# Optimization experiments

Measured on AMD Instinct MI355X. Metric: run time of the kernel, lower is better.

## Reference

```python
import jax, jax.numpy as jnp
import numpy as np

B, N, T = 32, 256, 1024  # batch, num_dimensions, time_dur


def setup_inputs() -> dict:
    key = jax.random.key(0)
    k1, k2 = jax.random.split(key)
    x = jax.random.normal(k1, (B, N, T), dtype=jnp.float32)
    # DBNN.__init__: tau_rise=50, tau_decay=200, omega=2 (all per-dimension)
    tau_rise = jnp.full((N,), 50.0, dtype=jnp.float32)
    tau_decay = jnp.full((N,), 200.0, dtype=jnp.float32)
    omega = jnp.full((N,), 2.0, dtype=jnp.float32)
    # BilinearModified weight: uniform(-1/sqrt(N), 1/sqrt(N)), shape [out=1, N, N]
    bound = 1.0 / np.sqrt(N)
    W = jax.random.uniform(k2, (1, N, N), minval=-bound, maxval=bound, dtype=jnp.float32)
    return {"x": x, "tau_rise": tau_rise, "tau_decay": tau_decay, "omega": omega, "W": W}


def reference(x, tau_rise, tau_decay, omega, W):
    B_, N_, T_ = x.shape
    BIAS = -70.0  # fixed bias buffer in BilinearModified

    # --- create_kernels: [N, T] exponential rise/decay kernels ---
    t = jnp.arange(T_, dtype=x.dtype)
    kernels = (omega[:, None]
               * (1.0 - jnp.exp(-t / tau_rise[:, None]))
               * jnp.exp(-t / tau_decay[:, None]))  # [N, T]

    # torch flips the kernel then runs cross-correlation (conv1d) => causal convolution
    k_flipped = jnp.flip(kernels, axis=-1)[:, None, :]  # [N, 1, T] (OIW, depthwise)

    y = jax.lax.conv_general_dilated(
        x, k_flipped,
        window_strides=(1,),
        padding=[(T_ - 1, T_ - 1)],
        dimension_numbers=("NCH", "OIH", "NCH"),
        feature_group_count=N_,
    )[:, :, :T_]  # [B, N, T]

    yt = jnp.transpose(y, (0, 2, 1))  # [B, T, N]

    # Bilinear with diagonal of weight zeroed (mask-multiply, equivalent to the
    # in-place diagonal-zeroing loop in the torch module)
    Wm = W * (1.0 - jnp.eye(N_, dtype=W.dtype))  # [1, N, N]
    bilinear = jnp.einsum("btn,onm,btm->bto", yt, Wm, yt)  # [B, T, 1]

    linear = jnp.sum(yt, axis=2, keepdims=True)  # [B, T, 1]
    out = bilinear + BIAS + linear
    return out[..., 0]  # [B, T]
```

## Files before the change

kernel.cpp:

```cpp
#include <hip/hip_runtime.h>

typedef _Float16 f16;
typedef _Float16 f16x4 __attribute__((ext_vector_type(4)));
typedef _Float16 f16x8 __attribute__((ext_vector_type(8)));
typedef float    f32x4 __attribute__((ext_vector_type(4)));

#define NB 32
#define ND 256
#define NT 1024

__global__ __launch_bounds__(256) void iir_wprep_kernel(
    const float* __restrict__ x, const float* __restrict__ tau_rise,
    const float* __restrict__ tau_decay, const float* __restrict__ omega,
    const float* __restrict__ W, f16* __restrict__ y16, f16* __restrict__ wf)
{
    if (blockIdx.x >= 2048) {
        const int gid  = (blockIdx.x - 2048) * 256 + threadIdx.x;
        const int ks8  = gid >> 10;
        const int nt   = (gid >> 6) & 15;
        const int lane = gid & 63;
        const int nrow = nt * 16 + (lane & 15);
        const int k0   = ks8 * 32 + (lane >> 4) * 8;
        f16x8 v;
        #pragma unroll
        for (int j = 0; j < 8; ++j) {
            int k = k0 + j;
            float w = W[nrow * 256 + k];
            v[j] = (f16)((k == nrow) ? 0.0f : w);
        }
        *reinterpret_cast<f16x8*>(wf + (size_t)gid * 8) = v;
        return;
    }

    const int lane = threadIdx.x & 63;
    const int wid  = threadIdx.x >> 6;
    const int row  = blockIdx.x * 4 + wid;
    const int n    = row & (ND - 1);

    const float td = tau_decay[n];
    const float tr = tau_rise[n];
    const float om = omega[n];
    const float ad = expf(-1.0f / td);
    const float am = expf(-(1.0f / tr + 1.0f / td));

    const float* xr = x + (size_t)row * NT + lane * 16;
    float xv[16];
    #pragma unroll
    for (int i = 0; i < 4; ++i) {
        f32x4 v = *reinterpret_cast<const f32x4*>(xr + i * 4);
        xv[i*4+0] = v[0]; xv[i*4+1] = v[1]; xv[i*4+2] = v[2]; xv[i*4+3] = v[3];
    }

    float ld[16], lm[16];
    float sd = 0.f, sm = 0.f;
    #pragma unroll
    for (int i = 0; i < 16; ++i) {
        sd = fmaf(ad, sd, xv[i]); ld[i] = sd;
        sm = fmaf(am, sm, xv[i]); lm[i] = sm;
    }

    float t2;
    t2 = ad * ad; t2 = t2 * t2; t2 = t2 * t2; const float a16d = t2 * t2;
    t2 = am * am; t2 = t2 * t2; t2 = t2 * t2; const float a16m = t2 * t2;

    float Xd = sd, Xm = sm;
    float wdp = a16d, wmp = a16m;
    #pragma unroll
    for (int off = 1; off < 64; off <<= 1) {
        float pd = __shfl_up(Xd, off);
        float pm = __shfl_up(Xm, off);
        if (lane >= off) { Xd = fmaf(wdp, pd, Xd); Xm = fmaf(wmp, pm, Xm); }
        wdp *= wdp; wmp *= wmp;
    }
    float cd = __shfl_up(Xd, 1);
    float cm = __shfl_up(Xm, 1);
    if (lane == 0) { cd = 0.f; cm = 0.f; }

    f16x8 o0, o1;
    float pd = ad, pm = am;
    #pragma unroll
    for (int i = 0; i < 16; ++i) {
        float yd = fmaf(pd, cd, ld[i]);
        float ym = fmaf(pm, cm, lm[i]);
        float yv = om * (yd - ym);
        if (i < 8) o0[i] = (f16)yv; else o1[i - 8] = (f16)yv;
        pd *= ad; pm *= am;
    }
    f16* dst = y16 + (size_t)row * NT + lane * 16;
    *reinterpret_cast<f16x8*>(dst)     = o0;
    *reinterpret_cast<f16x8*>(dst + 8) = o1;
}

__global__ __launch_bounds__(512, 4) void bilinear_kernel(
    const f16* __restrict__ y16, const f16* __restrict__ wf,
    float* __restrict__ out)
{
    __shared__ __align__(16) f16 Yl[16384];
    __shared__ float sbuf[8][64];

    const int bi = blockIdx.x;
    const int tt = bi & 15;
    const int b  = bi >> 4;
    const int t0 = tt * 64;
    const int tid = threadIdx.x;

    {
        const int m    = tid & 255;
        const int half = tid >> 8;
        const f16* ysrc = y16 + ((size_t)(b * ND + m)) * NT + t0 + half * 32;
        f16x8 vy[4];
        #pragma unroll
        for (int c = 0; c < 4; ++c)
            vy[c] = *reinterpret_cast<const f16x8*>(ysrc + c * 8);
        #pragma unroll
        for (int c = 0; c < 4; ++c) {
            #pragma unroll
            for (int e = 0; e < 8; ++e) {
                int tl = half * 32 + c * 8 + e;
                Yl[tl * 256 + (m ^ (e << 3))] = vy[c][e];
            }
        }
    }
    __syncthreads();

    const int lane = tid & 63;
    const int w    = tid >> 6;
    const int g    = lane >> 4;

    int tl4[4], sw4[4];
    #pragma unroll
    for (int tf = 0; tf < 4; ++tf) {
        tl4[tf] = tf * 16 + (lane & 15);
        sw4[tf] = (tl4[tf] & 7) << 3;
    }

    f32x4 acc[2][4];
    #pragma unroll
    for (int a = 0; a < 2; ++a)
        #pragma unroll
        for (int tf = 0; tf < 4; ++tf) acc[a][tf] = (f32x4){0.f,0.f,0.f,0.f};

    #pragma unroll
    for (int ks = 0; ks < 8; ++ks) {
        f16x8 afrag[2];
        #pragma unroll
        for (int a = 0; a < 2; ++a)
            afrag[a] = *reinterpret_cast<const f16x8*>(
                &wf[(size_t)(((ks * 16) + (2 * w + a)) * 64 + lane) * 8]);
        f16x8 bfrag[4];
        #pragma unroll
        for (int tf = 0; tf < 4; ++tf) {
            int m0 = ks * 32 + g * 8;
            bfrag[tf] = *reinterpret_cast<const f16x8*>(
                &Yl[tl4[tf] * 256 + (m0 ^ sw4[tf])]);
        }
        #pragma unroll
        for (int a = 0; a < 2; ++a)
            #pragma unroll
            for (int tf = 0; tf < 4; ++tf)
                acc[a][tf] = __builtin_amdgcn_mfma_f32_16x16x32_f16(
                    afrag[a], bfrag[tf], acc[a][tf], 0, 0, 0);
    }

    #pragma unroll
    for (int tf = 0; tf < 4; ++tf) {
        float p = 0.f;
        #pragma unroll
        for (int a = 0; a < 2; ++a) {
            int n0 = w * 32 + a * 16 + g * 4;
            f16x4 yv4 = *reinterpret_cast<const f16x4*>(
                &Yl[tl4[tf] * 256 + (n0 ^ sw4[tf])]);
            #pragma unroll
            for (int r = 0; r < 4; ++r)
                p = fmaf((float)yv4[r], acc[a][tf][r] + 1.0f, p);
        }
        p += __shfl_xor(p, 16);
        p += __shfl_xor(p, 32);
        if (lane < 16) sbuf[w][tf * 16 + lane] = p;
    }
    __syncthreads();
    if (tid < 64) {
        float s = sbuf[0][tid] + sbuf[1][tid] + sbuf[2][tid] + sbuf[3][tid]
                + sbuf[4][tid] + sbuf[5][tid] + sbuf[6][tid] + sbuf[7][tid];
        out[b * NT + t0 + tid] = s - 70.0f;
    }
}

extern "C" void kernel_launch(void* const* d_in, const int* in_sizes, int n_in,
                              void* d_out, int out_size, void* d_ws, size_t ws_size,
                              hipStream_t stream) {
    const float* x         = (const float*)d_in[0];
    const float* tau_rise  = (const float*)d_in[1];
    const float* tau_decay = (const float*)d_in[2];
    const float* omega     = (const float*)d_in[3];
    const float* W         = (const float*)d_in[4];
    float* out = (float*)d_out;

    f16* y16 = (f16*)d_ws;
    f16* wfr = (f16*)((char*)d_ws + (size_t)16 * 1024 * 1024);

    iir_wprep_kernel<<<2048 + 32, 256, 0, stream>>>(
        x, tau_rise, tau_decay, omega, W, y16, wfr);
    bilinear_kernel<<<NB * 16, 512, 0, stream>>>(y16, wfr, out);
}
```

Baseline: 24.08 us.

## Store scan checkpoints and recompute filtered signal inside bilinear kernel

The first kernel now writes only per-32-step IIR carry checkpoints instead of the full fp16 filtered tensor. The bilinear kernel rereads x in fp32, restarts the recurrence from each checkpoint, and writes the fp16 result straight into shared memory. This drops the 16 MB y16 write and its reread, but x (32 MB) is now read twice. It also adds a 32-step serial recurrence per thread inside the bilinear kernel, with scalar, bank-conflicting shared stores.

```diff
diff --git a/kernel.cpp b/kernel.cpp
--- a/kernel.cpp
+++ b/kernel.cpp
@@ -9,10 +9,11 @@
 #define ND 256
 #define NT 1024
 
-__global__ __launch_bounds__(256) void iir_wprep_kernel(
+__global__ __launch_bounds__(256) void scan_chk_wprep_kernel(
     const float* __restrict__ x, const float* __restrict__ tau_rise,
     const float* __restrict__ tau_decay, const float* __restrict__ omega,
-    const float* __restrict__ W, f16* __restrict__ y16, f16* __restrict__ wf)
+    const float* __restrict__ W, float2* __restrict__ chk,
+    f16* __restrict__ wf)
 {
     if (blockIdx.x >= 2048) {
         const int gid  = (blockIdx.x - 2048) * 256 + threadIdx.x;
@@ -37,62 +38,47 @@
     const int row  = blockIdx.x * 4 + wid;
     const int n    = row & (ND - 1);
 
-    const float td = tau_decay[n];
-    const float tr = tau_rise[n];
-    const float om = omega[n];
-    const float ad = expf(-1.0f / td);
-    const float am = expf(-(1.0f / tr + 1.0f / td));
+    const float ad = expf(-1.0f / tau_decay[n]);
+    const float am = expf(-(1.0f / tau_rise[n] + 1.0f / tau_decay[n]));
 
     const float* xr = x + (size_t)row * NT + lane * 16;
-    float xv[16];
-    #pragma unroll
-    for (int i = 0; i < 4; ++i) {
-        f32x4 v = *reinterpret_cast<const f32x4*>(xr + i * 4);
-        xv[i*4+0] = v[0]; xv[i*4+1] = v[1]; xv[i*4+2] = v[2]; xv[i*4+3] = v[3];
-    }
-
-    float ld[16], lm[16];
+    f32x4 v0 = *reinterpret_cast<const f32x4*>(xr);
+    f32x4 v1 = *reinterpret_cast<const f32x4*>(xr + 4);
+    f32x4 v2 = *reinterpret_cast<const f32x4*>(xr + 8);
+    f32x4 v3 = *reinterpret_cast<const f32x4*>(xr + 12);
+
     float sd = 0.f, sm = 0.f;
     #pragma unroll
-    for (int i = 0; i < 16; ++i) {
-        sd = fmaf(ad, sd, xv[i]); ld[i] = sd;
-        sm = fmaf(am, sm, xv[i]); lm[i] = sm;
-    }
+    for (int i = 0; i < 4; ++i) { sd = fmaf(ad, sd, v0[i]); sm = fmaf(am, sm, v0[i]); }
+    #pragma unroll
+    for (int i = 0; i < 4; ++i) { sd = fmaf(ad, sd, v1[i]); sm = fmaf(am, sm, v1[i]); }
+    #pragma unroll
+    for (int i = 0; i < 4; ++i) { sd = fmaf(ad, sd, v2[i]); sm = fmaf(am, sm, v2[i]); }
+    #pragma unroll
+    for (int i = 0; i < 4; ++i) { sd = fmaf(ad, sd, v3[i]); sm = fmaf(am, sm, v3[i]); }
 
     float t2;
-    t2 = ad * ad; t2 = t2 * t2; t2 = t2 * t2; const float a16d = t2 * t2;
-    t2 = am * am; t2 = t2 * t2; t2 = t2 * t2; const float a16m = t2 * t2;
+    t2 = ad * ad; t2 = t2 * t2; t2 = t2 * t2; float wd = t2 * t2;
+    t2 = am * am; t2 = t2 * t2; t2 = t2 * t2; float wm = t2 * t2;
 
     float Xd = sd, Xm = sm;
-    float wdp = a16d, wmp = a16m;
     #pragma unroll
     for (int off = 1; off < 64; off <<= 1) {
         float pd = __shfl_up(Xd, off);
         float pm = __shfl_up(Xm, off);
-        if (lane >= off) { Xd = fmaf(wdp, pd, Xd); Xm = fmaf(wmp, pm, Xm); }
-        wdp *= wdp; wmp *= wmp;
-    }
-    float cd = __shfl_up(Xd, 1);
-    float cm = __shfl_up(Xm, 1);
-    if (lane == 0) { cd = 0.f; cm = 0.f; }
-
-    f16x8 o0, o1;
-    float pd = ad, pm = am;
-    #pragma unroll
-    for (int i = 0; i < 16; ++i) {
-        float yd = fmaf(pd, cd, ld[i]);
-        float ym = fmaf(pm, cm, lm[i]);
-        float yv = om * (yd - ym);
-        if (i < 8) o0[i] = (f16)yv; else o1[i - 8] = (f16)yv;
-        pd *= ad; pm *= am;
-    }
-    f16* dst = y16 + (size_t)row * NT + lane * 16;
-    *reinterpret_cast<f16x8*>(dst)     = o0;
-    *reinterpret_cast<f16x8*>(dst + 8) = o1;
+        if (lane >= off) { Xd = fmaf(wd, pd, Xd); Xm = fmaf(wm, pm, Xm); }
+        wd *= wd; wm *= wm;
+    }
+
+    float2* cr = chk + (size_t)row * 32;
+    if (lane == 0) cr[0] = make_float2(0.f, 0.f);
+    if ((lane & 1) && lane < 63) cr[(lane + 1) >> 1] = make_float2(Xd, Xm);
 }
 
 __global__ __launch_bounds__(512, 4) void bilinear_kernel(
-    const f16* __restrict__ y16, const f16* __restrict__ wf,
+    const float* __restrict__ x, const float* __restrict__ tau_rise,
+    const float* __restrict__ tau_decay, const float* __restrict__ omega,
+    const float2* __restrict__ chk, const f16* __restrict__ wf,
     float* __restrict__ out)
 {
     __shared__ __align__(16) f16 Yl[16384];
@@ -105,27 +91,36 @@
     const int tid = threadIdx.x;
 
     {
-        const int m    = tid & 255;
-        const int half = tid >> 8;
-        const f16* ysrc = y16 + ((size_t)(b * ND + m)) * NT + t0 + half * 32;
-        f16x8 vy[4];
-        #pragma unroll
-        for (int c = 0; c < 4; ++c)
-            vy[c] = *reinterpret_cast<const f16x8*>(ysrc + c * 8);
-        #pragma unroll
-        for (int c = 0; c < 4; ++c) {
-            #pragma unroll
-            for (int e = 0; e < 8; ++e) {
-                int tl = half * 32 + c * 8 + e;
-                Yl[tl * 256 + (m ^ (e << 3))] = vy[c][e];
-            }
+        const int m = tid >> 1;
+        const int h = tid & 1;
+        const int rowg = b * ND + m;
+        const float ad = expf(-1.0f / tau_decay[m]);
+        const float am = expf(-(1.0f / tau_rise[m] + 1.0f / tau_decay[m]));
+        const float om = omega[m];
+
+        const float* xs = x + (size_t)rowg * NT + t0 + h * 32;
+        f32x4 xv[8];
+        #pragma unroll
+        for (int c = 0; c < 8; ++c)
+            xv[c] = *reinterpret_cast<const f32x4*>(xs + c * 4);
+
+        float2 ck = chk[(size_t)rowg * 32 + tt * 2 + h];
+        float Sd = ck.x, Sm = ck.y;
+        #pragma unroll
+        for (int i = 0; i < 32; ++i) {
+            float xi = xv[i >> 2][i & 3];
+            Sd = fmaf(ad, Sd, xi);
+            Sm = fmaf(am, Sm, xi);
+            float yv = om * (Sd - Sm);
+            int tl = h * 32 + i;
+            Yl[tl * 256 + (m ^ ((tl & 7) << 3))] = (f16)yv;
         }
     }
     __syncthreads();
 
     const int lane = tid & 63;
     const int w    = tid >> 6;
-    const int g    = lane >> 4;
+    const int gq   = lane >> 4;
 
     int tl4[4], sw4[4];
     #pragma unroll
@@ -150,7 +145,7 @@
         f16x8 bfrag[4];
         #pragma unroll
         for (int tf = 0; tf < 4; ++tf) {
-            int m0 = ks * 32 + g * 8;
+            int m0 = ks * 32 + gq * 8;
             bfrag[tf] = *reinterpret_cast<const f16x8*>(
                 &Yl[tl4[tf] * 256 + (m0 ^ sw4[tf])]);
         }
@@ -167,7 +162,7 @@
         float p = 0.f;
         #pragma unroll
         for (int a = 0; a < 2; ++a) {
-            int n0 = w * 32 + a * 16 + g * 4;
+            int n0 = w * 32 + a * 16 + gq * 4;
             f16x4 yv4 = *reinterpret_cast<const f16x4*>(
                 &Yl[tl4[tf] * 256 + (n0 ^ sw4[tf])]);
             #pragma unroll
@@ -196,10 +191,11 @@
     const float* W         = (const float*)d_in[4];
     float* out = (float*)d_out;
 
-    f16* y16 = (f16*)d_ws;
-    f16* wfr = (f16*)((char*)d_ws + (size_t)16 * 1024 * 1024);
-
-    iir_wprep_kernel<<<2048 + 32, 256, 0, stream>>>(
-        x, tau_rise, tau_decay, omega, W, y16, wfr);
-    bilinear_kernel<<<NB * 16, 512, 0, stream>>>(y16, wfr, out);
+    float2* chk = (float2*)d_ws;
+    f16*    wfr = (f16*)((char*)d_ws + (size_t)4 * 1024 * 1024);
+
+    scan_chk_wprep_kernel<<<2048 + 32, 256, 0, stream>>>(
+        x, tau_rise, tau_decay, omega, W, chk, wfr);
+    bilinear_kernel<<<NB * 16, 512, 0, stream>>>(
+        x, tau_rise, tau_decay, omega, chk, wfr, out);
 }
```

After: 24.37 us. Within noise of the previous version (+1.2%).

## Halve bilinear block size, widen per-wave tiles, double-buffer W fragments

Applied to the files above, without the earlier changes.

The bilinear kernel now runs 256 threads per block instead of 512. Each wave computes four 16-row W tiles instead of two, so each Y fragment read from LDS is reused across more MFMAs. The W fragment global loads are double-buffered, prefetching the next k-slice while the current one is multiplied. The Y tile is now staged with 4-wide f16x4 LDS stores that gather four rows per thread. The cost is higher register pressure and fewer waves per block, which may reduce latency hiding.

```diff
diff --git a/kernel.cpp b/kernel.cpp
--- a/kernel.cpp
+++ b/kernel.cpp
@@ -91,12 +91,12 @@
     *reinterpret_cast<f16x8*>(dst + 8) = o1;
 }
 
-__global__ __launch_bounds__(512, 4) void bilinear_kernel(
+__global__ __launch_bounds__(256, 2) void bilinear_kernel(
     const f16* __restrict__ y16, const f16* __restrict__ wf,
     float* __restrict__ out)
 {
     __shared__ __align__(16) f16 Yl[16384];
-    __shared__ float sbuf[8][64];
+    __shared__ float sbuf[4][64];
 
     const int bi = blockIdx.x;
     const int tt = bi & 15;
@@ -105,27 +105,32 @@
     const int tid = threadIdx.x;
 
     {
-        const int m    = tid & 255;
-        const int half = tid >> 8;
-        const f16* ysrc = y16 + ((size_t)(b * ND + m)) * NT + t0 + half * 32;
-        f16x8 vy[4];
-        #pragma unroll
-        for (int c = 0; c < 4; ++c)
-            vy[c] = *reinterpret_cast<const f16x8*>(ysrc + c * 8);
-        #pragma unroll
-        for (int c = 0; c < 4; ++c) {
-            #pragma unroll
-            for (int e = 0; e < 8; ++e) {
-                int tl = half * 32 + c * 8 + e;
-                Yl[tl * 256 + (m ^ (e << 3))] = vy[c][e];
-            }
+        const int j2 = tid & 63;
+        const int h  = tid >> 6;
+        const f16* base = y16 + ((size_t)(b * ND + 4 * j2)) * NT + t0 + h * 16;
+        f16x8 vy[4][2];
+        #pragma unroll
+        for (int r = 0; r < 4; ++r) {
+            vy[r][0] = *reinterpret_cast<const f16x8*>(base + (size_t)r * NT);
+            vy[r][1] = *reinterpret_cast<const f16x8*>(base + (size_t)r * NT + 8);
+        }
+        #pragma unroll
+        for (int i = 0; i < 16; ++i) {
+            const int tl = h * 16 + i;
+            f16x4 v4;
+            v4[0] = vy[0][i >> 3][i & 7];
+            v4[1] = vy[1][i >> 3][i & 7];
+            v4[2] = vy[2][i >> 3][i & 7];
+            v4[3] = vy[3][i >> 3][i & 7];
+            *reinterpret_cast<f16x4*>(
+                &Yl[tl * 256 + ((4 * j2) ^ ((tl & 7) << 3))]) = v4;
         }
     }
     __syncthreads();
 
     const int lane = tid & 63;
     const int w    = tid >> 6;
-    const int g    = lane >> 4;
+    const int gq   = lane >> 4;
 
     int tl4[4], sw4[4];
     #pragma unroll
@@ -134,40 +139,70 @@
         sw4[tf] = (tl4[tf] & 7) << 3;
     }
 
-    f32x4 acc[2][4];
-    #pragma unroll
-    for (int a = 0; a < 2; ++a)
+    f32x4 acc[4][4];
+    #pragma unroll
+    for (int a = 0; a < 4; ++a)
         #pragma unroll
         for (int tf = 0; tf < 4; ++tf) acc[a][tf] = (f32x4){0.f,0.f,0.f,0.f};
 
-    #pragma unroll
-    for (int ks = 0; ks < 8; ++ks) {
-        f16x8 afrag[2];
-        #pragma unroll
-        for (int a = 0; a < 2; ++a)
-            afrag[a] = *reinterpret_cast<const f16x8*>(
-                &wf[(size_t)(((ks * 16) + (2 * w + a)) * 64 + lane) * 8]);
-        f16x8 bfrag[4];
-        #pragma unroll
-        for (int tf = 0; tf < 4; ++tf) {
-            int m0 = ks * 32 + g * 8;
-            bfrag[tf] = *reinterpret_cast<const f16x8*>(
-                &Yl[tl4[tf] * 256 + (m0 ^ sw4[tf])]);
-        }
-        #pragma unroll
-        for (int a = 0; a < 2; ++a)
-            #pragma unroll
-            for (int tf = 0; tf < 4; ++tf)
-                acc[a][tf] = __builtin_amdgcn_mfma_f32_16x16x32_f16(
-                    afrag[a], bfrag[tf], acc[a][tf], 0, 0, 0);
+    const f16* wbase = wf + (size_t)(4 * w) * 512 + (size_t)lane * 8;
+
+    f16x8 aA[4], aB[4];
+    #pragma unroll
+    for (int a_ = 0; a_ < 4; ++a_)
+        aA[a_] = *reinterpret_cast<const f16x8*>(wbase + (size_t)a_ * 512);
+
+    #pragma unroll
+    for (int kp = 0; kp < 4; ++kp) {
+        const int ks0 = 2 * kp, ks1 = 2 * kp + 1;
+        #pragma unroll
+        for (int a_ = 0; a_ < 4; ++a_)
+            aB[a_] = *reinterpret_cast<const f16x8*>(
+                wbase + (size_t)(ks1 * 16 + a_) * 512);
+        {
+            f16x8 bfrag[4];
+            #pragma unroll
+            for (int tf = 0; tf < 4; ++tf) {
+                int m0 = ks0 * 32 + gq * 8;
+                bfrag[tf] = *reinterpret_cast<const f16x8*>(
+                    &Yl[tl4[tf] * 256 + (m0 ^ sw4[tf])]);
+            }
+            #pragma unroll
+            for (int a = 0; a < 4; ++a)
+                #pragma unroll
+                for (int tf = 0; tf < 4; ++tf)
+                    acc[a][tf] = __builtin_amdgcn_mfma_f32_16x16x32_f16(
+                        aA[a], bfrag[tf], acc[a][tf], 0, 0, 0);
+        }
+        if (kp < 3) {
+            #pragma unroll
+            for (int a_ = 0; a_ < 4; ++a_)
+                aA[a_] = *reinterpret_cast<const f16x8*>(
+                    wbase + (size_t)((ks1 + 1) * 16 + a_) * 512);
+        }
+        {
+            f16x8 bfrag[4];
+            #pragma unroll
+            for (int tf = 0; tf < 4; ++tf) {
+                int m0 = ks1 * 32 + gq * 8;
+                bfrag[tf] = *reinterpret_cast<const f16x8*>(
+                    &Yl[tl4[tf] * 256 + (m0 ^ sw4[tf])]);
+            }
+            #pragma unroll
+            for (int a = 0; a < 4; ++a)
+                #pragma unroll
+                for (int tf = 0; tf < 4; ++tf)
+                    acc[a][tf] = __builtin_amdgcn_mfma_f32_16x16x32_f16(
+                        aB[a], bfrag[tf], acc[a][tf], 0, 0, 0);
+        }
     }
 
     #pragma unroll
     for (int tf = 0; tf < 4; ++tf) {
         float p = 0.f;
         #pragma unroll
-        for (int a = 0; a < 2; ++a) {
-            int n0 = w * 32 + a * 16 + g * 4;
+        for (int a = 0; a < 4; ++a) {
+            int n0 = 64 * w + 16 * a + 4 * gq;
             f16x4 yv4 = *reinterpret_cast<const f16x4*>(
                 &Yl[tl4[tf] * 256 + (n0 ^ sw4[tf])]);
             #pragma unroll
@@ -180,8 +215,7 @@
     }
     __syncthreads();
     if (tid < 64) {
-        float s = sbuf[0][tid] + sbuf[1][tid] + sbuf[2][tid] + sbuf[3][tid]
-                + sbuf[4][tid] + sbuf[5][tid] + sbuf[6][tid] + sbuf[7][tid];
+        float s = sbuf[0][tid] + sbuf[1][tid] + sbuf[2][tid] + sbuf[3][tid];
         out[b * NT + t0 + tid] = s - 70.0f;
     }
 }
@@ -201,5 +235,5 @@
 
     iir_wprep_kernel<<<2048 + 32, 256, 0, stream>>>(
         x, tau_rise, tau_decay, omega, W, y16, wfr);
-    bilinear_kernel<<<NB * 16, 512, 0, stream>>>(y16, wfr, out);
+    bilinear_kernel<<<NB * 16, 256, 0, stream>>>(y16, wfr, out);
 }
```

Result: slower. 24.99 us (+3.8%).
